# Kernel optimization log

Measured on AMD Instinct MI355X. Metric: run time of the kernel, lower is better.

The kernel has to match this reference:

```python
import jax, jax.numpy as jnp
import numpy as np

N = 25600   # total nodes
B = 256     # graphs / batch_size / LSTM seq length
F = 128     # num_feat
H = 256     # gnn_hidden
R = 512     # rnn_hidden == 2*H (forced by alm layer)
L = 2       # rnn_layers
V = 32000   # vocab
E = 409600  # edges
NPG = 100   # nodes per graph (forced by alm layer / attention reshape)


def setup_inputs() -> dict:
    key = jax.random.key(0)
    ks = jax.random.split(key, 20)
    def rn(k, shape, fan_in, scale=1.0):
        return jax.random.normal(k, shape, jnp.float32) * (scale / np.sqrt(fan_in))
    inp = {}
    inp['x'] = jax.random.normal(ks[0], (N, F), jnp.float32)
    inp['edge_index'] = jax.random.randint(ks[1], (2, E), 0, N)
    inp['bwd_edge_index'] = jnp.flip(inp['edge_index'], axis=0)
    inp['batch'] = jnp.arange(N) // NPG  # contiguous graphs, 100 nodes each
    inp['h0'] = jax.random.normal(ks[2], (L, 1, R), jnp.float32)
    inp['c0'] = jax.random.normal(ks[3], (L, 1, R), jnp.float32)
    inp['W_gnn'] = rn(ks[4], (F, H), F)
    inp['W_root'] = rn(ks[5], (H, H), H)
    inp['W_nbr'] = rn(ks[6], (H, H), H)
    inp['b_conv'] = jnp.zeros((H,), jnp.float32)
    D = 2 * H
    inp['W1'] = rn(ks[7], (D, D), D); inp['b1'] = jnp.zeros((D,), jnp.float32)
    inp['gamma'] = jnp.ones((D,), jnp.float32); inp['beta'] = jnp.zeros((D,), jnp.float32)
    inp['W2'] = rn(ks[8], (D, D), D); inp['b2'] = jnp.zeros((D,), jnp.float32)
    A = NPG * R + R  # alm input dim = rnn_hidden*100 + rnn_hidden
    inp['W_alm'] = rn(ks[9], (NPG, A), A, scale=0.1)
    inp['b_alm'] = jnp.ones((NPG,), jnp.float32)  # keeps alpha.sum() well away from 0
    inp['Wih0'] = rn(ks[10], (4 * R, D), D); inp['Whh0'] = rn(ks[11], (4 * R, R), R)
    inp['bih0'] = jnp.zeros((4 * R,), jnp.float32); inp['bhh0'] = jnp.zeros((4 * R,), jnp.float32)
    inp['Wih1'] = rn(ks[12], (4 * R, R), R); inp['Whh1'] = rn(ks[13], (4 * R, R), R)
    inp['bih1'] = jnp.zeros((4 * R,), jnp.float32); inp['bhh1'] = jnp.zeros((4 * R,), jnp.float32)
    inp['W_fc'] = rn(ks[14], (R, V), R); inp['b_fc'] = jnp.zeros((V,), jnp.float32)
    return inp


def _lstm_layer(inputs, h, c, Wih, Whh, bih, bhh):
    # inputs: (T, 1, in); carry h, c: (1, R). PyTorch gate order i, f, g, o.
    def step(carry, xt):
        h, c = carry
        g = xt @ Wih.T + bih + h @ Whh.T + bhh
        i, f, gg, o = jnp.split(g, 4, axis=-1)
        c = jax.nn.sigmoid(f) * c + jax.nn.sigmoid(i) * jnp.tanh(gg)
        h = jax.nn.sigmoid(o) * jnp.tanh(c)
        return (h, c), h
    (hT, cT), outs = jax.lax.scan(step, (h, c), inputs)
    return outs, hT, cT


def reference(x, edge_index, bwd_edge_index, batch, h0, c0, W_gnn, W_root, W_nbr, b_conv,
              W1, b1, gamma, beta, W2, b2, W_alm, b_alm,
              Wih0, Whh0, bih0, bhh0, Wih1, Whh1, bih1, bhh1, W_fc, b_fc):
    n = x.shape[0]
    x = x @ W_gnn  # (N, H)
    # GraphConv: out_i = W_root x_i + W_nbr * sum_{j->i} x_j + b.
    # (Original loops gnn_layers times from the SAME x, so only the last conv matters.)
    def conv(xx, ei):
        agg = jax.ops.segment_sum(xx[ei[0]], ei[1], num_segments=n)
        return xx @ W_root + agg @ W_nbr + b_conv
    fwd_x = jax.nn.relu(conv(x, edge_index))
    bwd_x = jax.nn.relu(conv(x, bwd_edge_index))
    xc = jnp.concatenate([fwd_x, bwd_x], axis=1)  # (N, 2H) == (N, R)
    # MLP [2H, 2H, 2H]: Lin -> BatchNorm(batch stats) -> ReLU -> (dropout off) -> Lin
    h1 = xc @ W1 + b1
    h1 = (h1 - h1.mean(0)) / jnp.sqrt(h1.var(0) + 1e-5) * gamma + beta
    x_mlp = jax.nn.relu(h1) @ W2 + b2
    # global mean pool over graphs
    counts = jax.ops.segment_sum(jnp.ones((n,), x_mlp.dtype), batch, num_segments=B)
    x_g = jax.ops.segment_sum(x_mlp, batch, num_segments=B) / counts[:, None]
    x_emb = x_g.reshape(B, 1, 2 * H)  # LSTM: seq_len=B, batch=1
    # attention over cell state (vectorized form of the nested loops):
    # alpha[l,b,:] = alm(cat(c0[l].flatten(), h3[b].flatten())); normalize by sum (NOT softmax);
    # new_c[l] = sum_b alpha[l,b,:] @ h3[b]
    h3 = xc.reshape(B, NPG, R)
    s = c0.reshape(L, R)
    Ws, Wh = W_alm[:, :R], W_alm[:, R:]
    alpha = (s @ Ws.T)[:, None, :] + (h3.reshape(B, NPG * R) @ Wh.T)[None] + b_alm  # (L,B,NPG)
    alpha = alpha / alpha.sum(-1, keepdims=True)
    new_c = jnp.einsum('lbk,bkd->ld', alpha, h3)  # (L, R)
    # 2-layer LSTM (eval mode: inter-layer dropout is identity)
    outs, hT0, cT0 = _lstm_layer(x_emb, h0[0], new_c[0:1], Wih0, Whh0, bih0, bhh0)
    outs, hT1, cT1 = _lstm_layer(outs, h0[1], new_c[1:2], Wih1, Whh1, bih1, bhh1)
    preds = (outs @ W_fc + b_fc)[:, -1, :]  # (B, V)
    return preds
```

## Files before the change

kernel.cpp:

```cpp
#include <hip/hip_runtime.h>
#include <math.h>

#define N_NODES 25600
#define F_IN    128
#define H_GNN   256
#define D_MLP   512
#define E_EDGE  409600
#define B_GR    256
#define NPG_    100
#define R_LSTM  512
#define V_OUT   32000

typedef __bf16 bf16x8 __attribute__((ext_vector_type(8)));
typedef float  f32x4  __attribute__((ext_vector_type(4)));
typedef unsigned short u16x8 __attribute__((ext_vector_type(8)));

__device__ __forceinline__ unsigned short f2bf(float x) {
    unsigned u = __builtin_bit_cast(unsigned, x);
    unsigned r = (u + 0x7FFFu + ((u >> 16) & 1u)) >> 16;
    return (unsigned short)r;
}

template<bool TRANSB>
__global__ __launch_bounds__(256)
void gemm_tile(const float* __restrict__ A, const float* __restrict__ B,
               float* __restrict__ C, const float* __restrict__ bias,
               int M, int N, int K, int lda, int ldb, int ldc, int kChunk)
{
    __shared__ float As[16][68];
    __shared__ float Bs[16][68];
    const int tid = threadIdx.x;
    const int n0 = blockIdx.x * 64;
    const int m0 = blockIdx.y * 64;
    const int z  = blockIdx.z;
    const int k0 = z * kChunk;
    const int k1 = min(K, k0 + kChunk);
    const int ty = tid >> 4, tx = tid & 15;
    float acc[4][4] = {};

    for (int kb = k0; kb < k1; kb += 16) {
        {
            const int r = tid >> 4, c = tid & 15;
            #pragma unroll
            for (int i = 0; i < 4; ++i) {
                int rr = r + i * 16;
                int gm = m0 + rr, gk = kb + c;
                As[c][rr] = (gm < M && gk < k1) ? A[gm * lda + gk] : 0.f;
            }
        }
        if (!TRANSB) {
            const int r = tid >> 6, c = tid & 63;
            #pragma unroll
            for (int i = 0; i < 4; ++i) {
                int rr = r + i * 4;
                int gk = kb + rr, gn = n0 + c;
                Bs[rr][c] = (gk < k1 && gn < N) ? B[gk * ldb + gn] : 0.f;
            }
        } else {
            const int r = tid & 15, c = tid >> 4;
            #pragma unroll
            for (int i = 0; i < 4; ++i) {
                int cc = c + i * 16;
                int gk = kb + r, gn = n0 + cc;
                Bs[r][cc] = (gk < k1 && gn < N) ? B[gn * ldb + gk] : 0.f;
            }
        }
        __syncthreads();
        #pragma unroll
        for (int kk = 0; kk < 16; ++kk) {
            float a[4], b[4];
            #pragma unroll
            for (int i = 0; i < 4; ++i) a[i] = As[kk][ty * 4 + i];
            #pragma unroll
            for (int j = 0; j < 4; ++j) b[j] = Bs[kk][tx * 4 + j];
            #pragma unroll
            for (int i = 0; i < 4; ++i)
                #pragma unroll
                for (int j = 0; j < 4; ++j)
                    acc[i][j] = fmaf(a[i], b[j], acc[i][j]);
        }
        __syncthreads();
    }

    const bool split = (gridDim.z > 1);
    #pragma unroll
    for (int i = 0; i < 4; ++i) {
        int gm = m0 + ty * 4 + i;
        if (gm >= M) continue;
        #pragma unroll
        for (int j = 0; j < 4; ++j) {
            int gn = n0 + tx * 4 + j;
            if (gn >= N) continue;
            float v = acc[i][j];
            if (bias != nullptr && z == 0) v += bias[gn];
            if (split) atomicAdd(&C[gm * ldc + gn], v);
            else       C[gm * ldc + gn] = v;
        }
    }
}

__global__ __launch_bounds__(256)
void gemm_f32_big(const float* __restrict__ A, const float* __restrict__ B,
                  float* __restrict__ C, const float* __restrict__ bias,
                  int M, int N, int K, int lda, int ldb, int ldc)
{
    __shared__ float As[8][128];
    __shared__ float Bs[8][128];
    const int tid = threadIdx.x;
    const int tx = tid & 15, ty = tid >> 4;
    const int n0 = blockIdx.x * 128, m0 = blockIdx.y * 128;
    float acc[8][8] = {};

    for (int kb = 0; kb < K; kb += 8) {
        {
            int r = tid >> 1, c = (tid & 1) * 4;
            float4 v = *(const float4*)(A + (long)(m0 + r) * lda + kb + c);
            As[c + 0][r] = v.x; As[c + 1][r] = v.y;
            As[c + 2][r] = v.z; As[c + 3][r] = v.w;
        }
        {
            int r = tid >> 5, c = (tid & 31) * 4;
            *(float4*)&Bs[r][c] = *(const float4*)(B + (long)(kb + r) * ldb + n0 + c);
        }
        __syncthreads();
        #pragma unroll
        for (int kk = 0; kk < 8; ++kk) {
            float a[8], b[8];
            *(float4*)&a[0] = *(const float4*)&As[kk][ty * 8];
            *(float4*)&a[4] = *(const float4*)&As[kk][ty * 8 + 4];
            *(float4*)&b[0] = *(const float4*)&Bs[kk][tx * 8];
            *(float4*)&b[4] = *(const float4*)&Bs[kk][tx * 8 + 4];
            #pragma unroll
            for (int i = 0; i < 8; ++i)
                #pragma unroll
                for (int j = 0; j < 8; ++j)
                    acc[i][j] = fmaf(a[i], b[j], acc[i][j]);
        }
        __syncthreads();
    }

    #pragma unroll
    for (int i = 0; i < 8; ++i) {
        int gm = m0 + ty * 8 + i;
        #pragma unroll
        for (int j = 0; j < 8; j += 4) {
            int gn = n0 + tx * 8 + j;
            float4 v = {acc[i][j], acc[i][j+1], acc[i][j+2], acc[i][j+3]};
            if (bias != nullptr) {
                v.x += bias[gn]; v.y += bias[gn + 1];
                v.z += bias[gn + 2]; v.w += bias[gn + 3];
            }
            *(float4*)(C + (long)gm * ldc + gn) = v;
        }
    }
}

__global__ __launch_bounds__(256)
void mfma_gemm(const unsigned short* __restrict__ A,
               const unsigned short* __restrict__ Bt,
               float* __restrict__ C, const float* __restrict__ bias,
               int M, int N, int K, int lda, int ldb, int ldc, int kChunk)
{
    __shared__ unsigned short As[128][40];
    __shared__ unsigned short Bs[128][40];
    const int tid  = threadIdx.x;
    const int lane = tid & 63;
    const int wv   = tid >> 6;
    const int wr   = wv >> 1, wc = wv & 1;
    const int n0 = blockIdx.x * 128;
    const int m0 = blockIdx.y * 128;
    const int z  = blockIdx.z;
    const int k0 = z * kChunk;
    const int k1 = min(K, k0 + kChunk);

    const int srow = tid >> 2;
    const int skoff = (tid & 3) * 8;

    f32x4 acc[4][4] = {};

    for (int kb = k0; kb < k1; kb += 32) {
        #pragma unroll
        for (int p = 0; p < 2; ++p) {
            int row = p * 64 + srow;
            u16x8 va = *(const u16x8*)(A + (long)(m0 + row) * lda + kb + skoff);
            *(u16x8*)&As[row][skoff] = va;
            int gb = n0 + row;
            u16x8 vb = {0, 0, 0, 0, 0, 0, 0, 0};
            if (gb < N) vb = *(const u16x8*)(Bt + (long)gb * ldb + kb + skoff);
            *(u16x8*)&Bs[row][skoff] = vb;
        }
        __syncthreads();
        bf16x8 af[4], bfr[4];
        #pragma unroll
        for (int fm = 0; fm < 4; ++fm)
            af[fm] = *(const bf16x8*)&As[wr * 64 + fm * 16 + (lane & 15)][(lane >> 4) * 8];
        #pragma unroll
        for (int fn = 0; fn < 4; ++fn)
            bfr[fn] = *(const bf16x8*)&Bs[wc * 64 + fn * 16 + (lane & 15)][(lane >> 4) * 8];
        #pragma unroll
        for (int fm = 0; fm < 4; ++fm)
            #pragma unroll
            for (int fn = 0; fn < 4; ++fn)
                acc[fm][fn] = __builtin_amdgcn_mfma_f32_16x16x32_bf16(
                    af[fm], bfr[fn], acc[fm][fn], 0, 0, 0);
        __syncthreads();
    }

    const bool split = (gridDim.z > 1);
    #pragma unroll
    for (int fm = 0; fm < 4; ++fm) {
        int row = m0 + wr * 64 + fm * 16 + ((lane >> 4) << 2);
        #pragma unroll
        for (int fn = 0; fn < 4; ++fn) {
            int col = n0 + wc * 64 + fn * 16 + (lane & 15);
            if (col >= N) continue;
            f32x4 v = acc[fm][fn];
            #pragma unroll
            for (int r = 0; r < 4; ++r) {
                float o = v[r];
                if (bias != nullptr && z == 0) o += bias[col];
                if (split) atomicAdd(&C[(long)(row + r) * ldc + col], o);
                else       C[(long)(row + r) * ldc + col] = o;
            }
        }
    }
}

__global__ void castbf(const float* __restrict__ in, unsigned short* __restrict__ out,
                       long n) {
    long stride = (long)gridDim.x * blockDim.x * 4;
    for (long j = ((long)blockIdx.x * blockDim.x + threadIdx.x) * 4; j < n; j += stride) {
        float4 v = *(const float4*)(in + j);
        ushort4 o;
        o.x = f2bf(v.x); o.y = f2bf(v.y); o.z = f2bf(v.z); o.w = f2bf(v.w);
        *(ushort4*)(out + j) = o;
    }
}
__global__ void cast_strided(const float* __restrict__ in, unsigned short* __restrict__ out,
                             int cols, long ldin, long off) {
    const int r = blockIdx.y;
    int c = (blockIdx.x * blockDim.x + threadIdx.x) * 4;
    if (c < cols) {
        float4 v = *(const float4*)(in + (long)r * ldin + off + c);
        ushort4 o;
        o.x = f2bf(v.x); o.y = f2bf(v.y); o.z = f2bf(v.z); o.w = f2bf(v.w);
        *(ushort4*)(out + (long)r * cols + c) = o;
    }
}
__global__ __launch_bounds__(256)
void transcast(const float* __restrict__ in, unsigned short* __restrict__ out,
               int R, int C) {
    __shared__ unsigned short t[64][72];
    const int c0 = blockIdx.x * 64, r0 = blockIdx.y * 64;
    const int tid = threadIdx.x;
    const int rr = tid >> 2, cg = (tid & 3) * 16;
    #pragma unroll
    for (int i = 0; i < 4; ++i) {
        float4 v = *(const float4*)(in + (long)(r0 + rr) * C + c0 + cg + i * 4);
        t[cg + i * 4 + 0][rr] = f2bf(v.x);
        t[cg + i * 4 + 1][rr] = f2bf(v.y);
        t[cg + i * 4 + 2][rr] = f2bf(v.z);
        t[cg + i * 4 + 3][rr] = f2bf(v.w);
    }
    __syncthreads();
    const int cc = tid >> 2, kg = (tid & 3) * 16;
    #pragma unroll
    for (int i = 0; i < 2; ++i) {
        u16x8 v = *(const u16x8*)&t[cc][kg + i * 8];
        *(u16x8*)(out + (long)(c0 + cc) * R + r0 + kg + i * 8) = v;
    }
}

__global__ void zero_i32(int* p, long n) {
    for (long i = (long)blockIdx.x * blockDim.x + threadIdx.x; i < n;
         i += (long)gridDim.x * blockDim.x) p[i] = 0;
}
__global__ __launch_bounds__(256)
void prep_kernel(const float* __restrict__ bih0, const float* __restrict__ bhh0,
                 const float* __restrict__ bih1, const float* __restrict__ bhh1,
                 const float* __restrict__ b_conv, const float* __restrict__ c0,
                 const float* __restrict__ W_alm,
                 float* b0s, float* b1s, float* bc2, float* sW,
                 float* colsum, float* colsq, float* newc, float* hW) {
    const int b = blockIdx.x, t = threadIdx.x;
    if (b < 8) {
        int i = b * 256 + t;
        b0s[i] = bih0[i] + bhh0[i];
        b1s[i] = bih1[i] + bhh1[i];
    } else if (b == 8) {
        bc2[t] = b_conv[t];
        bc2[t + 256] = 0.f;
    } else if (b == 9) {
        if (t < 2 * NPG_) {
            int l = t / NPG_, p = t % NPG_;
            float s = 0.f;
            for (int k = 0; k < R_LSTM; ++k)
                s += c0[l * R_LSTM + k] * W_alm[(long)p * 51712 + k];
            sW[l * NPG_ + p] = s;
        }
    } else if (b == 10) {
        for (int i = t; i < 512; i += 256) { colsum[i] = 0.f; colsq[i] = 0.f; }
        for (int i = t; i < 1024; i += 256) newc[i] = 0.f;
    } else {
        int i = (b - 11) * 256 + t;
        if (i < 25600) hW[i] = 0.f;
    }
}

__global__ void hist2_kernel(const int* __restrict__ ei0, const int* __restrict__ ei1,
                             int* counts_d, int* counts_s, int E) {
    int i = blockIdx.x * blockDim.x + threadIdx.x;
    if (i < E) {
        atomicAdd(&counts_d[ei1[i]], 1);
        atomicAdd(&counts_s[ei0[i]], 1);
    }
}
__global__ __launch_bounds__(256)
void scan_chunk2(const int* __restrict__ counts_d, const int* __restrict__ counts_s,
                 int* rowptr_d, int* rowptr_s, int* tops_d, int* tops_s, int n) {
    __shared__ int buf[256];
    const int half = blockIdx.x >= 100;
    const int chunk = half ? blockIdx.x - 100 : blockIdx.x;
    const int* counts = half ? counts_s : counts_d;
    int* rowptr = half ? rowptr_s : rowptr_d;
    int* tops   = half ? tops_s   : tops_d;
    const int tid = threadIdx.x;
    int i = chunk * 256 + tid;
    int v = (i < n) ? counts[i] : 0;
    buf[tid] = v;
    __syncthreads();
    for (int off = 1; off < 256; off <<= 1) {
        int add = (tid >= off) ? buf[tid - off] : 0;
        __syncthreads();
        buf[tid] += add;
        __syncthreads();
    }
    if (i < n) rowptr[i + 1] = buf[tid];
    if (tid == 255) tops[chunk] = buf[255];
}
__global__ __launch_bounds__(128)
void scan_tops2(int* tops_d, int* tops_s, int nt) {
    __shared__ int b[128];
    int* tops = (blockIdx.x == 0) ? tops_d : tops_s;
    int tid = threadIdx.x;
    int v = (tid < nt) ? tops[tid] : 0;
    b[tid] = v;
    __syncthreads();
    for (int off = 1; off < 128; off <<= 1) {
        int add = (tid >= off) ? b[tid - off] : 0;
        __syncthreads();
        b[tid] += add;
        __syncthreads();
    }
    if (tid < nt) tops[tid] = b[tid] - v;
}
__global__ void scan_fixup2(const int* __restrict__ counts_d, const int* __restrict__ counts_s,
                            int* rowptr_d, int* rowptr_s,
                            int* cursor_d, int* cursor_s,
                            const int* __restrict__ tops_d, const int* __restrict__ tops_s,
                            int n) {
    const int half = blockIdx.x >= 100;
    const int chunk = half ? blockIdx.x - 100 : blockIdx.x;
    const int* counts = half ? counts_s : counts_d;
    const int* tops   = half ? tops_s   : tops_d;
    int* rowptr = half ? rowptr_s : rowptr_d;
    int* cursor = half ? cursor_s : cursor_d;
    int i = chunk * 256 + threadIdx.x;
    if (i < n) {
        int r = rowptr[i + 1] + tops[chunk];
        rowptr[i + 1] = r;
        cursor[i] = r - counts[i];
        if (i == 0) rowptr[0] = 0;
    }
}
__global__ void scatter2_kernel(const int* __restrict__ ei0, const int* __restrict__ ei1,
                                int* cursor_d, int* cursor_s,
                                int* sorted_d, int* sorted_s, int E) {
    int i = blockIdx.x * blockDim.x + threadIdx.x;
    if (i < E) {
        int s = ei0[i], d = ei1[i];
        int pd = atomicAdd(&cursor_d[d], 1);
        sorted_d[pd] = s;
        int ps = atomicAdd(&cursor_s[s], 1);
        sorted_s[ps] = d;
    }
}
__global__ __launch_bounds__(512)
void agg_conv2(const float* __restrict__ xrn,
               const int* __restrict__ rowptr_d, const int* __restrict__ sorted_d,
               const int* __restrict__ rowptr_s, const int* __restrict__ sorted_s,
               float* __restrict__ xc, unsigned short* __restrict__ xcb) {
    const int n = blockIdx.x;
    const int tid = threadIdx.x;
    const int c = tid & 255;
    const bool bwd = tid >= 256;
    const int* rowptr = bwd ? rowptr_s : rowptr_d;
    const int* sorted = bwd ? sorted_s : sorted_d;
    float acc = xrn[(long)n * 512 + c];
    const int s = rowptr[n], e = rowptr[n + 1];
    for (int t = s; t < e; ++t)
        acc += xrn[(long)sorted[t] * 512 + 256 + c];
    float r = fmaxf(acc, 0.f);
    long idx = (long)n * 512 + (bwd ? 256 : 0) + c;
    xc[idx] = r;
    xcb[idx] = f2bf(r);
}

__global__ __launch_bounds__(512)
void colstat_kernel(const float* __restrict__ h1, float* colsum, float* colsq) {
    const int c = threadIdx.x;
    const int r0 = blockIdx.x * 128;
    float s = 0.f, s2 = 0.f;
    for (int r = 0; r < 128; ++r) {
        float v = h1[(long)(r0 + r) * D_MLP + c];
        s += v; s2 += v * v;
    }
    atomicAdd(&colsum[c], s);
    atomicAdd(&colsq[c], s2);
}
__global__ void finalize_stats(const float* colsum, const float* colsq,
                               const float* gamma, const float* beta,
                               float* scalev, float* shiftv) {
    int c = threadIdx.x;
    float m  = colsum[c] * (1.f / N_NODES);
    float vr = colsq[c] * (1.f / N_NODES) - m * m;
    float g  = gamma[c] * rsqrtf(vr + 1e-5f);
    scalev[c] = g;
    shiftv[c] = beta[c] - m * g;
}
__global__ __launch_bounds__(512)
void fused_norm_pool(const float* __restrict__ h1, const float* __restrict__ sc,
                     const float* __restrict__ sh, float* __restrict__ P) {
    const int b = blockIdx.x, c = threadIdx.x;
    const float scv = sc[c], shv = sh[c];
    float s = 0.f;
    for (int i = 0; i < NPG_; ++i) {
        float v = h1[(long)(b * NPG_ + i) * D_MLP + c];
        s += fmaxf(fmaf(v, scv, shv), 0.f);
    }
    P[b * D_MLP + c] = s * (1.f / NPG_);
}
__global__ __launch_bounds__(128)
void alpha_kernel(const float* __restrict__ sW, const float* __restrict__ hW,
                  const float* __restrict__ b_alm, float* __restrict__ alpha) {
    const int lb = blockIdx.x;
    const int l = lb >> 8, b = lb & 255;
    const int p = threadIdx.x;
    __shared__ float red[128];
    float v = 0.f;
    if (p < NPG_) v = sW[l * NPG_ + p] + hW[b * NPG_ + p] + b_alm[p];
    red[p] = v;
    __syncthreads();
    for (int s = 64; s > 0; s >>= 1) {
        if (p < s) red[p] += red[p + s];
        __syncthreads();
    }
    float inv = 1.f / red[0];
    if (p < NPG_) alpha[lb * NPG_ + p] = v * inv;
}
__global__ __launch_bounds__(512)
void newc_kernel(const float* __restrict__ alpha, const float* __restrict__ xc,
                 float* new_c) {
    const int l = blockIdx.y, chunk = blockIdx.x, c = threadIdx.x;
    const int r0 = chunk * 800;
    float acc = 0.f;
    for (int r = r0; r < r0 + 800; ++r)
        acc += alpha[l * N_NODES + r] * xc[(long)r * D_MLP + c];
    atomicAdd(&new_c[l * D_MLP + c], acc);
}

#define CANARY 0x7FC00000u
#define SPIN_MAX 20000

__device__ __forceinline__ unsigned coh_load_u(const unsigned* p) {
    return __hip_atomic_load(p, __ATOMIC_RELAXED, __HIP_MEMORY_SCOPE_AGENT);
}
__device__ __forceinline__ void coh_store_f(float* p, float v) {
    __hip_atomic_store(p, v, __ATOMIC_RELAXED, __HIP_MEMORY_SCOPE_AGENT);
}

__global__ void lstm_init_kernel(const float* __restrict__ h0,
                                 float* h0buf, float* h1buf) {
    int i = blockIdx.x * blockDim.x + threadIdx.x;
    if (i < 512) { h0buf[i] = h0[i]; h1buf[i] = h0[512 + i]; }
    for (int j = 512 + i; j < 257 * 512; j += gridDim.x * blockDim.x) {
        ((unsigned*)h0buf)[j] = CANARY;
        ((unsigned*)h1buf)[j] = CANARY;
    }
}

__global__ __launch_bounds__(512)
void lstm_kernel(const float* __restrict__ inp0, const float* __restrict__ Whh0,
                 const float* __restrict__ Wih1, const float* __restrict__ Whh1,
                 const float* __restrict__ b1s, const float* __restrict__ new_c,
                 float* h0buf, float* h1buf)
{
    const int tid  = threadIdx.x;
    const int lane = tid & 63;
    const int w    = tid >> 6;
    const int blk  = blockIdx.x;
    const int layer = blk >> 5;
    const int base  = (blk & 31) * 16;
    const int gate  = lane >> 4;
    const int hid   = lane & 15;
    const int rowg  = gate * 512 + base + hid;

    __shared__ float partial[2][8][64];

    if (layer == 0) {
        float wr[64];
        {
            const float4* wp = (const float4*)(Whh0 + (long)rowg * 512 + w * 64);
            #pragma unroll
            for (int i = 0; i < 16; ++i) {
                float4 v = wp[i];
                wr[4*i] = v.x; wr[4*i+1] = v.y; wr[4*i+2] = v.z; wr[4*i+3] = v.w;
            }
        }
        float c = (w == 0 && lane < 16) ? new_c[base + lane] : 0.f;
        const unsigned* src = (const unsigned*)h0buf + w * 64 + lane;
        for (int t = 0; t < 256; ++t) {
            float ipv = (w == 0) ? inp0[t * 2048 + rowg] : 0.f;
            unsigned hu; int guard = 0;
            for (;;) {
                hu = coh_load_u(src + (long)t * 512);
                if (!__any(hu == CANARY)) break;
                if (++guard > SPIN_MAX) break;
                if (guard > 32) __builtin_amdgcn_s_sleep(1);
            }
            float hv = __uint_as_float(hu);
            float acc = 0.f;
            #pragma unroll
            for (int j = 0; j < 64; ++j)
                acc = fmaf(wr[j], __shfl(hv, j), acc);
            partial[t & 1][w][lane] = acc;
            __syncthreads();
            if (w == 0) {
                float g = ipv;
                #pragma unroll
                for (int ww = 0; ww < 8; ++ww) g += partial[t & 1][ww][lane];
                float a = (gate == 2) ? tanhf(g) : 1.f / (1.f + expf(-g));
                float fv = __shfl(a, lane + 16);
                float gv = __shfl(a, lane + 32);
                float ov = __shfl(a, lane + 48);
                if (lane < 16) {
                    c = fv * c + a * gv;
                    float h = ov * tanhf(c);
                    coh_store_f(h0buf + (long)(t + 1) * 512 + base + lane, h);
                }
            }
        }
    } else {
        const float* Wsel = (w < 4) ? Wih1 : Whh1;
        const int koff = (w & 3) * 128;
        float wrA[64], wrB[64];
        {
            const float4* wp = (const float4*)(Wsel + (long)rowg * 512 + koff);
            #pragma unroll
            for (int i = 0; i < 16; ++i) {
                float4 v = wp[i];
                wrA[4*i] = v.x; wrA[4*i+1] = v.y; wrA[4*i+2] = v.z; wrA[4*i+3] = v.w;
            }
            #pragma unroll
            for (int i = 0; i < 16; ++i) {
                float4 v = wp[16 + i];
                wrB[4*i] = v.x; wrB[4*i+1] = v.y; wrB[4*i+2] = v.z; wrB[4*i+3] = v.w;
            }
        }
        float bsum = (w == 0) ? b1s[rowg] : 0.f;
        float c = (w == 0 && lane < 16) ? new_c[512 + base + lane] : 0.f;
        for (int t = 0; t < 256; ++t) {
            const unsigned* xsrc = (w < 4)
                ? (const unsigned*)h0buf + (long)(t + 1) * 512 + koff
                : (const unsigned*)h1buf + (long)t * 512 + koff;
            unsigned hu0, hu1; int guard = 0;
            for (;;) {
                hu0 = coh_load_u(xsrc + lane);
                hu1 = coh_load_u(xsrc + 64 + lane);
                if (!__any((hu0 == CANARY) || (hu1 == CANARY))) break;
                if (++guard > SPIN_MAX) break;
                if (guard > 32) __builtin_amdgcn_s_sleep(1);
            }
            float hv0 = __uint_as_float(hu0), hv1 = __uint_as_float(hu1);
            float acc = 0.f;
            #pragma unroll
            for (int j = 0; j < 64; ++j)
                acc = fmaf(wrA[j], __shfl(hv0, j), acc);
            #pragma unroll
            for (int j = 0; j < 64; ++j)
                acc = fmaf(wrB[j], __shfl(hv1, j), acc);
            partial[t & 1][w][lane] = acc;
            __syncthreads();
            if (w == 0) {
                float g = bsum;
                #pragma unroll
                for (int ww = 0; ww < 8; ++ww) g += partial[t & 1][ww][lane];
                float a = (gate == 2) ? tanhf(g) : 1.f / (1.f + expf(-g));
                float fv = __shfl(a, lane + 16);
                float gv = __shfl(a, lane + 32);
                float ov = __shfl(a, lane + 48);
                if (lane < 16) {
                    c = fv * c + a * gv;
                    float h = ov * tanhf(c);
                    coh_store_f(h1buf + (long)(t + 1) * 512 + base + lane, h);
                }
            }
        }
    }
}

extern "C" void kernel_launch(void* const* d_in, const int* in_sizes, int n_in,
                              void* d_out, int out_size, void* d_ws, size_t ws_size,
                              hipStream_t stream)
{
    const float* x      = (const float*)d_in[0];
    const int*   ei     = (const int*)d_in[1];
    const float* h0     = (const float*)d_in[4];
    const float* c0     = (const float*)d_in[5];
    const float* W_gnn  = (const float*)d_in[6];
    const float* W_root = (const float*)d_in[7];
    const float* W_nbr  = (const float*)d_in[8];
    const float* b_conv = (const float*)d_in[9];
    const float* W1     = (const float*)d_in[10];
    const float* b1     = (const float*)d_in[11];
    const float* gamma  = (const float*)d_in[12];
    const float* beta   = (const float*)d_in[13];
    const float* W2     = (const float*)d_in[14];
    const float* b2     = (const float*)d_in[15];
    const float* W_alm  = (const float*)d_in[16];
    const float* b_alm  = (const float*)d_in[17];
    const float* Wih0   = (const float*)d_in[18];
    const float* Whh0   = (const float*)d_in[19];
    const float* bih0   = (const float*)d_in[20];
    const float* bhh0   = (const float*)d_in[21];
    const float* Wih1   = (const float*)d_in[22];
    const float* Whh1   = (const float*)d_in[23];
    const float* bih1   = (const float*)d_in[24];
    const float* bhh1   = (const float*)d_in[25];
    const float* W_fc   = (const float*)d_in[26];
    const float* b_fc   = (const float*)d_in[27];
    float* out = (float*)d_out;
    float* ws  = (float*)d_ws;

    const int* ei0 = ei;
    const int* ei1 = ei + E_EDGE;

    float* xrn = ws;
    float* h1m = ws;
    unsigned short* Wfct  = (unsigned short*)ws;
    unsigned short* Walmb = (unsigned short*)(ws + 8500000L);
    unsigned short* ob    = (unsigned short*)(ws + 11200000L);
    float* xc = ws + 13107200L;
    long o = 26214400L;
    float* Wc    = ws + o; o += 65536;
    int*   counts_d = (int*)(ws + o); o += 25600;
    int*   counts_s = (int*)(ws + o); o += 25600;
    int*   rowptr_d = (int*)(ws + o); o += 25601;
    int*   rowptr_s = (int*)(ws + o); o += 25601;
    int*   cursor_d = (int*)(ws + o); o += 25600;
    int*   cursor_s = (int*)(ws + o); o += 25600;
    int*   sorted_d = (int*)(ws + o); o += 409600;
    int*   sorted_s = (int*)(ws + o); o += 409600;
    int*   tops_d   = (int*)(ws + o); o += 128;
    int*   tops_s   = (int*)(ws + o); o += 128;
    float* colsum= ws + o; o += 512;
    float* colsq = ws + o; o += 512;
    float* scalev= ws + o; o += 512;
    float* shiftv= ws + o; o += 512;
    float* P     = ws + o; o += 131072;
    float* x_g   = ws + o; o += 131072;
    float* hW    = ws + o; o += 25600;
    float* sW    = ws + o; o += 200;
    float* alphav= ws + o; o += 51200;
    float* newc  = ws + o; o += 1024;
    float* b0s   = ws + o; o += 2048;
    float* b1s   = ws + o; o += 2048;
    float* bc2   = ws + o; o += 512;
    unsigned short* xcb = (unsigned short*)(ws + o);
    float* inp0  = ws + o;
    float* h0st  = ws + o + 524288;
    float* h1st  = ws + o + 655872;
    o += 6553600;

    prep_kernel<<<dim3(111), 256, 0, stream>>>(bih0, bhh0, bih1, bhh1, b_conv, c0,
                                               W_alm, b0s, b1s, bc2, sW,
                                               colsum, colsq, newc, hW);
    gemm_tile<false><<<dim3(4, 2, 1), 256, 0, stream>>>(W_gnn, W_root, Wc, nullptr,
        128, 256, 256, 256, 256, 512, 256);
    gemm_tile<false><<<dim3(4, 2, 1), 256, 0, stream>>>(W_gnn, W_nbr, Wc + 256, nullptr,
        128, 256, 256, 256, 256, 512, 256);
    gemm_f32_big<<<dim3(4, 200), 256, 0, stream>>>(x, Wc, xrn, bc2,
        N_NODES, 512, 128, 128, 512, 512);
    zero_i32<<<dim3(200), 256, 0, stream>>>(counts_d, 51200);
    hist2_kernel<<<dim3(1600), 256, 0, stream>>>(ei0, ei1, counts_d, counts_s, E_EDGE);
    scan_chunk2<<<dim3(200), 256, 0, stream>>>(counts_d, counts_s, rowptr_d, rowptr_s,
                                               tops_d, tops_s, 25600);
    scan_tops2<<<dim3(2), 128, 0, stream>>>(tops_d, tops_s, 100);
    scan_fixup2<<<dim3(200), 256, 0, stream>>>(counts_d, counts_s, rowptr_d, rowptr_s,
                                               cursor_d, cursor_s, tops_d, tops_s, 25600);
    scatter2_kernel<<<dim3(1600), 256, 0, stream>>>(ei0, ei1, cursor_d, cursor_s,
                                                    sorted_d, sorted_s, E_EDGE);
    agg_conv2<<<dim3(25600), 512, 0, stream>>>(xrn, rowptr_d, sorted_d,
                                               rowptr_s, sorted_s, xc, xcb);
    gemm_f32_big<<<dim3(4, 200), 256, 0, stream>>>(xc, W1, h1m, b1,
        N_NODES, 512, 512, 512, 512, 512);
    colstat_kernel<<<dim3(200), 512, 0, stream>>>(h1m, colsum, colsq);
    finalize_stats<<<dim3(1), 512, 0, stream>>>(colsum, colsq, gamma, beta, scalev, shiftv);
    fused_norm_pool<<<dim3(256), 512, 0, stream>>>(h1m, scalev, shiftv, P);
    gemm_tile<false><<<dim3(8, 4, 1), 256, 0, stream>>>(P, W2, x_g, b2,
        256, 512, 512, 512, 512, 512, 512);
    transcast<<<dim3(500, 8), 256, 0, stream>>>(W_fc, Wfct, 512, V_OUT);
    cast_strided<<<dim3(50, 100), 256, 0, stream>>>(W_alm, Walmb, 51200, 51712L, 512L);
    mfma_gemm<<<dim3(1, 2, 100), 256, 0, stream>>>(xcb, Walmb, hW, nullptr,
        256, 100, 51200, 51200, 51200, 100, 512);
    alpha_kernel<<<dim3(512), 128, 0, stream>>>(sW, hW, b_alm, alphav);
    newc_kernel<<<dim3(32, 2), 512, 0, stream>>>(alphav, xc, newc);
    gemm_tile<true><<<dim3(32, 4, 1), 256, 0, stream>>>(x_g, Wih0, inp0, b0s,
        256, 2048, 512, 512, 512, 2048, 512);
    lstm_init_kernel<<<dim3(64), 512, 0, stream>>>(h0, h0st, h1st);
    lstm_kernel<<<dim3(64), 512, 0, stream>>>(inp0, Whh0, Wih1, Whh1, b1s, newc,
                                              h0st, h1st);
    castbf<<<dim3(128), 256, 0, stream>>>(h1st + 512, ob, 131072L);
    mfma_gemm<<<dim3(250, 2, 1), 256, 0, stream>>>(ob, Wfct, out, b_fc,
        256, V_OUT, 512, 512, 512, V_OUT, 512);
}
```

Baseline: 1.894 ms.

## Fuse small kernels, deepen f32 GEMM K-tile, and write bf16 LSTM output directly

Folds several small launches into neighbouring kernels. Zeroing the counts moves into prep_kernel, the top-level scan moves into scan_fixup2, finalize_stats moves into fused_norm_pool, and the bf16 cast of the LSTM output is now written by lstm_kernel itself. newc_kernel handles both layers in one pass so xc is read once, and gemm_f32_big doubles its K-step to 16 so it synchronises half as often. These changes cut launch overhead and redundant memory traffic, at the cost of a serial prefix loop in each fixup block and a larger shared-memory footprint in the GEMM.

Result: no change. 1.903 ms (median of 2 runs) (+0.5%).

```diff
diff --git a/kernel.cpp b/kernel.cpp
--- a/kernel.cpp
+++ b/kernel.cpp
@@ -104,27 +104,31 @@
                   float* __restrict__ C, const float* __restrict__ bias,
                   int M, int N, int K, int lda, int ldb, int ldc)
 {
-    __shared__ float As[8][128];
-    __shared__ float Bs[8][128];
+    __shared__ float As[16][128];
+    __shared__ float Bs[16][128];
     const int tid = threadIdx.x;
     const int tx = tid & 15, ty = tid >> 4;
     const int n0 = blockIdx.x * 128, m0 = blockIdx.y * 128;
     float acc[8][8] = {};
 
-    for (int kb = 0; kb < K; kb += 8) {
+    for (int kb = 0; kb < K; kb += 16) {
         {
-            int r = tid >> 1, c = (tid & 1) * 4;
-            float4 v = *(const float4*)(A + (long)(m0 + r) * lda + kb + c);
-            As[c + 0][r] = v.x; As[c + 1][r] = v.y;
-            As[c + 2][r] = v.z; As[c + 3][r] = v.w;
+            int r = tid >> 1, cb = (tid & 1) * 8;
+            float4 v0 = *(const float4*)(A + (long)(m0 + r) * lda + kb + cb);
+            float4 v1 = *(const float4*)(A + (long)(m0 + r) * lda + kb + cb + 4);
+            As[cb + 0][r] = v0.x; As[cb + 1][r] = v0.y;
+            As[cb + 2][r] = v0.z; As[cb + 3][r] = v0.w;
+            As[cb + 4][r] = v1.x; As[cb + 5][r] = v1.y;
+            As[cb + 6][r] = v1.z; As[cb + 7][r] = v1.w;
         }
         {
-            int r = tid >> 5, c = (tid & 31) * 4;
-            *(float4*)&Bs[r][c] = *(const float4*)(B + (long)(kb + r) * ldb + n0 + c);
-        }
-        __syncthreads();
-        #pragma unroll
-        for (int kk = 0; kk < 8; ++kk) {
+            int r = tid >> 4, cb = (tid & 15) * 8;
+            *(float4*)&Bs[r][cb]     = *(const float4*)(B + (long)(kb + r) * ldb + n0 + cb);
+            *(float4*)&Bs[r][cb + 4] = *(const float4*)(B + (long)(kb + r) * ldb + n0 + cb + 4);
+        }
+        __syncthreads();
+        #pragma unroll
+        for (int kk = 0; kk < 16; ++kk) {
             float a[8], b[8];
             *(float4*)&a[0] = *(const float4*)&As[kk][ty * 8];
             *(float4*)&a[4] = *(const float4*)&As[kk][ty * 8 + 4];
@@ -226,16 +230,6 @@
     }
 }
 
-__global__ void castbf(const float* __restrict__ in, unsigned short* __restrict__ out,
-                       long n) {
-    long stride = (long)gridDim.x * blockDim.x * 4;
-    for (long j = ((long)blockIdx.x * blockDim.x + threadIdx.x) * 4; j < n; j += stride) {
-        float4 v = *(const float4*)(in + j);
-        ushort4 o;
-        o.x = f2bf(v.x); o.y = f2bf(v.y); o.z = f2bf(v.z); o.w = f2bf(v.w);
-        *(ushort4*)(out + j) = o;
-    }
-}
 __global__ void cast_strided(const float* __restrict__ in, unsigned short* __restrict__ out,
                              int cols, long ldin, long off) {
     const int r = blockIdx.y;
@@ -271,17 +265,14 @@
     }
 }
 
-__global__ void zero_i32(int* p, long n) {
-    for (long i = (long)blockIdx.x * blockDim.x + threadIdx.x; i < n;
-         i += (long)gridDim.x * blockDim.x) p[i] = 0;
-}
 __global__ __launch_bounds__(256)
 void prep_kernel(const float* __restrict__ bih0, const float* __restrict__ bhh0,
                  const float* __restrict__ bih1, const float* __restrict__ bhh1,
                  const float* __restrict__ b_conv, const float* __restrict__ c0,
                  const float* __restrict__ W_alm,
                  float* b0s, float* b1s, float* bc2, float* sW,
-                 float* colsum, float* colsq, float* newc, float* hW) {
+                 float* colsum, float* colsq, float* newc, float* hW,
+                 int* counts) {
     const int b = blockIdx.x, t = threadIdx.x;
     if (b < 8) {
         int i = b * 256 + t;
@@ -301,9 +292,12 @@
     } else if (b == 10) {
         for (int i = t; i < 512; i += 256) { colsum[i] = 0.f; colsq[i] = 0.f; }
         for (int i = t; i < 1024; i += 256) newc[i] = 0.f;
-    } else {
+    } else if (b < 111) {
         int i = (b - 11) * 256 + t;
         if (i < 25600) hW[i] = 0.f;
+    } else {
+        int i = (b - 111) * 256 + t;
+        if (i < 51200) counts[i] = 0;
     }
 }
 
@@ -338,36 +332,28 @@
     if (i < n) rowptr[i + 1] = buf[tid];
     if (tid == 255) tops[chunk] = buf[255];
 }
-__global__ __launch_bounds__(128)
-void scan_tops2(int* tops_d, int* tops_s, int nt) {
-    __shared__ int b[128];
-    int* tops = (blockIdx.x == 0) ? tops_d : tops_s;
-    int tid = threadIdx.x;
-    int v = (tid < nt) ? tops[tid] : 0;
-    b[tid] = v;
-    __syncthreads();
-    for (int off = 1; off < 128; off <<= 1) {
-        int add = (tid >= off) ? b[tid - off] : 0;
-        __syncthreads();
-        b[tid] += add;
-        __syncthreads();
-    }
-    if (tid < nt) tops[tid] = b[tid] - v;
-}
-__global__ void scan_fixup2(const int* __restrict__ counts_d, const int* __restrict__ counts_s,
-                            int* rowptr_d, int* rowptr_s,
-                            int* cursor_d, int* cursor_s,
-                            const int* __restrict__ tops_d, const int* __restrict__ tops_s,
-                            int n) {
+__global__ __launch_bounds__(256)
+void scan_fixup2(const int* __restrict__ counts_d, const int* __restrict__ counts_s,
+                 int* rowptr_d, int* rowptr_s,
+                 int* cursor_d, int* cursor_s,
+                 const int* __restrict__ tops_d, const int* __restrict__ tops_s,
+                 int n) {
     const int half = blockIdx.x >= 100;
     const int chunk = half ? blockIdx.x - 100 : blockIdx.x;
     const int* counts = half ? counts_s : counts_d;
     const int* tops   = half ? tops_s   : tops_d;
     int* rowptr = half ? rowptr_s : rowptr_d;
     int* cursor = half ? cursor_s : cursor_d;
+    __shared__ int base_s;
+    if (threadIdx.x == 0) {
+        int b = 0;
+        for (int j = 0; j < chunk; ++j) b += tops[j];
+        base_s = b;
+    }
+    __syncthreads();
     int i = chunk * 256 + threadIdx.x;
     if (i < n) {
-        int r = rowptr[i + 1] + tops[chunk];
+        int r = rowptr[i + 1] + base_s;
         rowptr[i + 1] = r;
         cursor[i] = r - counts[i];
         if (i == 0) rowptr[0] = 0;
@@ -418,21 +404,16 @@
     atomicAdd(&colsum[c], s);
     atomicAdd(&colsq[c], s2);
 }
-__global__ void finalize_stats(const float* colsum, const float* colsq,
-                               const float* gamma, const float* beta,
-                               float* scalev, float* shiftv) {
-    int c = threadIdx.x;
+__global__ __launch_bounds__(512)
+void fused_norm_pool(const float* __restrict__ h1,
+                     const float* __restrict__ colsum, const float* __restrict__ colsq,
+                     const float* __restrict__ gamma, const float* __restrict__ beta,
+                     float* __restrict__ P) {
+    const int b = blockIdx.x, c = threadIdx.x;
     float m  = colsum[c] * (1.f / N_NODES);
     float vr = colsq[c] * (1.f / N_NODES) - m * m;
-    float g  = gamma[c] * rsqrtf(vr + 1e-5f);
-    scalev[c] = g;
-    shiftv[c] = beta[c] - m * g;
-}
-__global__ __launch_bounds__(512)
-void fused_norm_pool(const float* __restrict__ h1, const float* __restrict__ sc,
-                     const float* __restrict__ sh, float* __restrict__ P) {
-    const int b = blockIdx.x, c = threadIdx.x;
-    const float scv = sc[c], shv = sh[c];
+    float scv = gamma[c] * rsqrtf(vr + 1e-5f);
+    float shv = beta[c] - m * scv;
     float s = 0.f;
     for (int i = 0; i < NPG_; ++i) {
         float v = h1[(long)(b * NPG_ + i) * D_MLP + c];
@@ -461,12 +442,16 @@
 __global__ __launch_bounds__(512)
 void newc_kernel(const float* __restrict__ alpha, const float* __restrict__ xc,
                  float* new_c) {
-    const int l = blockIdx.y, chunk = blockIdx.x, c = threadIdx.x;
+    const int chunk = blockIdx.x, c = threadIdx.x;
     const int r0 = chunk * 800;
-    float acc = 0.f;
-    for (int r = r0; r < r0 + 800; ++r)
-        acc += alpha[l * N_NODES + r] * xc[(long)r * D_MLP + c];
-    atomicAdd(&new_c[l * D_MLP + c], acc);
+    float a0 = 0.f, a1 = 0.f;
+    for (int r = r0; r < r0 + 800; ++r) {
+        float v = xc[(long)r * D_MLP + c];
+        a0 = fmaf(alpha[r], v, a0);
+        a1 = fmaf(alpha[N_NODES + r], v, a1);
+    }
+    atomicAdd(&new_c[c], a0);
+    atomicAdd(&new_c[512 + c], a1);
 }
 
 #define CANARY 0x7FC00000u
@@ -493,7 +478,7 @@
 void lstm_kernel(const float* __restrict__ inp0, const float* __restrict__ Whh0,
                  const float* __restrict__ Wih1, const float* __restrict__ Whh1,
                  const float* __restrict__ b1s, const float* __restrict__ new_c,
-                 float* h0buf, float* h1buf)
+                 float* h0buf, float* h1buf, unsigned short* __restrict__ ob)
 {
     const int tid  = threadIdx.x;
     const int lane = tid & 63;
@@ -603,6 +588,7 @@
                     c = fv * c + a * gv;
                     float h = ov * tanhf(c);
                     coh_store_f(h1buf + (long)(t + 1) * 512 + base + lane, h);
+                    ob[t * 512 + base + lane] = f2bf(h);
                 }
             }
         }
@@ -665,8 +651,6 @@
     int*   tops_s   = (int*)(ws + o); o += 128;
     float* colsum= ws + o; o += 512;
     float* colsq = ws + o; o += 512;
-    float* scalev= ws + o; o += 512;
-    float* shiftv= ws + o; o += 512;
     float* P     = ws + o; o += 131072;
     float* x_g   = ws + o; o += 131072;
     float* hW    = ws + o; o += 25600;
@@ -682,20 +666,18 @@
     float* h1st  = ws + o + 655872;
     o += 6553600;
 
-    prep_kernel<<<dim3(111), 256, 0, stream>>>(bih0, bhh0, bih1, bhh1, b_conv, c0,
+    prep_kernel<<<dim3(311), 256, 0, stream>>>(bih0, bhh0, bih1, bhh1, b_conv, c0,
                                                W_alm, b0s, b1s, bc2, sW,
-                                               colsum, colsq, newc, hW);
+                                               colsum, colsq, newc, hW, counts_d);
     gemm_tile<false><<<dim3(4, 2, 1), 256, 0, stream>>>(W_gnn, W_root, Wc, nullptr,
         128, 256, 256, 256, 256, 512, 256);
     gemm_tile<false><<<dim3(4, 2, 1), 256, 0, stream>>>(W_gnn, W_nbr, Wc + 256, nullptr,
         128, 256, 256, 256, 256, 512, 256);
     gemm_f32_big<<<dim3(4, 200), 256, 0, stream>>>(x, Wc, xrn, bc2,
         N_NODES, 512, 128, 128, 512, 512);
-    zero_i32<<<dim3(200), 256, 0, stream>>>(counts_d, 51200);
     hist2_kernel<<<dim3(1600), 256, 0, stream>>>(ei0, ei1, counts_d, counts_s, E_EDGE);
     scan_chunk2<<<dim3(200), 256, 0, stream>>>(counts_d, counts_s, rowptr_d, rowptr_s,
                                                tops_d, tops_s, 25600);
-    scan_tops2<<<dim3(2), 128, 0, stream>>>(tops_d, tops_s, 100);
     scan_fixup2<<<dim3(200), 256, 0, stream>>>(counts_d, counts_s, rowptr_d, rowptr_s,
                                                cursor_d, cursor_s, tops_d, tops_s, 25600);
     scatter2_kernel<<<dim3(1600), 256, 0, stream>>>(ei0, ei1, cursor_d, cursor_s,
@@ -705,8 +687,7 @@
     gemm_f32_big<<<dim3(4, 200), 256, 0, stream>>>(xc, W1, h1m, b1,
         N_NODES, 512, 512, 512, 512, 512);
     colstat_kernel<<<dim3(200), 512, 0, stream>>>(h1m, colsum, colsq);
-    finalize_stats<<<dim3(1), 512, 0, stream>>>(colsum, colsq, gamma, beta, scalev, shiftv);
-    fused_norm_pool<<<dim3(256), 512, 0, stream>>>(h1m, scalev, shiftv, P);
+    fused_norm_pool<<<dim3(256), 512, 0, stream>>>(h1m, colsum, colsq, gamma, beta, P);
     gemm_tile<false><<<dim3(8, 4, 1), 256, 0, stream>>>(P, W2, x_g, b2,
         256, 512, 512, 512, 512, 512, 512);
     transcast<<<dim3(500, 8), 256, 0, stream>>>(W_fc, Wfct, 512, V_OUT);
@@ -714,13 +695,12 @@
     mfma_gemm<<<dim3(1, 2, 100), 256, 0, stream>>>(xcb, Walmb, hW, nullptr,
         256, 100, 51200, 51200, 51200, 100, 512);
     alpha_kernel<<<dim3(512), 128, 0, stream>>>(sW, hW, b_alm, alphav);
-    newc_kernel<<<dim3(32, 2), 512, 0, stream>>>(alphav, xc, newc);
+    newc_kernel<<<dim3(32), 512, 0, stream>>>(alphav, xc, newc);
     gemm_tile<true><<<dim3(32, 4, 1), 256, 0, stream>>>(x_g, Wih0, inp0, b0s,
         256, 2048, 512, 512, 512, 2048, 512);
     lstm_init_kernel<<<dim3(64), 512, 0, stream>>>(h0, h0st, h1st);
     lstm_kernel<<<dim3(64), 512, 0, stream>>>(inp0, Whh0, Wih1, Whh1, b1s, newc,
-                                              h0st, h1st);
-    castbf<<<dim3(128), 256, 0, stream>>>(h1st + 512, ob, 131072L);
+                                              h0st, h1st, ob);
     mfma_gemm<<<dim3(250, 2, 1), 256, 0, stream>>>(ob, Wfct, out, b_fc,
         256, V_OUT, 512, 512, 512, V_OUT, 512);
 }
```
